# Performance work log

Hardware: AMD Instinct MI355X
Metric: run time of the kernel (lower is better)

The kernel has to match this reference:

```python
import jax, jax.numpy as jnp
import numpy as np

EPS = 1e-5

def _conv(x, w, b):
    # stride-2, pad-1 3x3 conv, NCHW / OIHW
    y = jax.lax.conv_general_dilated(x, w, (2, 2), [(1, 1), (1, 1)],
                                     dimension_numbers=('NCHW', 'OIHW', 'NCHW'))
    return y + b[None, :, None, None]

def _bn(x, gamma, beta):
    # training-mode batchnorm: batch statistics over (N,H,W), biased variance
    mu = x.mean(axis=(0, 2, 3), keepdims=True)
    var = x.var(axis=(0, 2, 3), keepdims=True)
    return gamma[None, :, None, None] * (x - mu) * jax.lax.rsqrt(var + EPS) + beta[None, :, None, None]

def setup_inputs():
    key = jax.random.key(0)
    ks = iter(jax.random.split(key, 40))
    def rn(shape, scale=0.05):
        return jax.random.normal(next(ks), shape, dtype=jnp.float32) * scale
    d = {}
    d['img'] = jax.random.normal(next(ks), (64, 3, 75, 75), dtype=jnp.float32)
    d['qst'] = jax.random.normal(next(ks), (64, 11), dtype=jnp.float32)
    # conv stack 3->32->64->128->256
    d['w1'] = rn((32, 3, 3, 3));    d['b1'] = jnp.zeros((32,), jnp.float32)
    d['w2'] = rn((64, 32, 3, 3));   d['b2'] = jnp.zeros((64,), jnp.float32)
    d['w3'] = rn((128, 64, 3, 3));  d['b3'] = jnp.zeros((128,), jnp.float32)
    d['w4'] = rn((256, 128, 3, 3)); d['b4'] = jnp.zeros((256,), jnp.float32)
    for i, c in zip((1, 2, 3, 4), (32, 64, 128, 256)):
        d[f'g{i}'] = jnp.ones((c,), jnp.float32)
        d[f'be{i}'] = jnp.zeros((c,), jnp.float32)
    # g MLP (torch Linear weights are [out,in])
    d['gw1'] = rn((2000, 523)); d['gb1'] = jnp.zeros((2000,), jnp.float32)
    d['gw2'] = rn((2000, 2000)); d['gb2'] = jnp.zeros((2000,), jnp.float32)
    d['gw3'] = rn((2000, 2000)); d['gb3'] = jnp.zeros((2000,), jnp.float32)
    d['gw4'] = rn((2000, 2000)); d['gb4'] = jnp.zeros((2000,), jnp.float32)
    # f MLP
    d['fw1'] = rn((1000, 2000)); d['fb1'] = jnp.zeros((1000,), jnp.float32)
    d['fw2'] = rn((500, 1000));  d['fb2'] = jnp.zeros((500,), jnp.float32)
    d['fw3'] = rn((100, 500));   d['fb3'] = jnp.zeros((100,), jnp.float32)
    d['fw4'] = rn((10, 100));    d['fb4'] = jnp.zeros((10,), jnp.float32)
    return d

def reference(img, qst, w1, b1, w2, b2, w3, b3, w4, b4,
              g1, be1, g2, be2, g3, be3, g4, be4,
              gw1, gb1, gw2, gb2, gw3, gb3, gw4, gb4,
              fw1, fb1, fw2, fb2, fw3, fb3, fw4, fb4):
    x = jax.nn.relu(_bn(_conv(img, w1, b1), g1, be1))
    x = jax.nn.relu(_bn(_conv(x, w2, b2), g2, be2))
    x = jax.nn.relu(_bn(_conv(x, w3, b3), g3, be3))
    x = jax.nn.relu(_bn(_conv(x, w4, b4), g4, be4))   # [B,256,5,5]
    B = x.shape[0]
    obj = x.reshape(B, 256, 25).transpose(0, 2, 1)     # [B,25,256], row-major like the loop
    oi = jnp.broadcast_to(obj[:, :, None, :], (B, 25, 25, 256))
    oj = jnp.broadcast_to(obj[:, None, :, :], (B, 25, 25, 256))
    q = jnp.broadcast_to(qst[:, None, None, :], (B, 25, 25, 11))
    pairs = jnp.concatenate([oi, oj, q], axis=-1).reshape(B * 625, 523)
    h = jax.nn.relu(pairs @ gw1.T + gb1)
    h = jax.nn.relu(h @ gw2.T + gb2)
    h = jax.nn.relu(h @ gw3.T + gb3)
    h = jax.nn.relu(h @ gw4.T + gb4)
    x_g = h.reshape(B, 625, 2000).sum(axis=1) / 625.0
    x_f = jax.nn.relu(x_g @ fw1.T + fb1)
    x_f = jax.nn.relu(x_f @ fw2.T + fb2)
    x_f = jax.nn.relu(x_f @ fw3.T + fb3)
    x_f = x_f @ fw4.T + fb4
    return jax.nn.log_softmax(x_f, axis=-1)
```

## Files before the change

kernel.cpp:

```cpp
#include <hip/hip_runtime.h>

typedef unsigned short u16;
typedef unsigned int u32;
typedef __attribute__((ext_vector_type(8))) short bf16x8;
typedef __attribute__((ext_vector_type(4))) float f32x4;

#define BN_EPS 1e-5f
#define BN_S 16

__device__ __forceinline__ float bf2f(u16 u) {
  union { unsigned u; float f; } x; x.u = ((unsigned)u) << 16; return x.f;
}
__device__ __forceinline__ u16 f2bf(float f) {
  union { float f; unsigned u; } x; x.f = f;
  unsigned r = x.u + 0x7FFFu + ((x.u >> 16) & 1u);
  return (u16)(r >> 16);
}

__global__ __launch_bounds__(256) void conv1_lds(const float* __restrict__ img,
                                                 const float* __restrict__ w,
                                                 const float* __restrict__ b,
                                                 float* __restrict__ C1) {
  int blk = blockIdx.x;
  int n = blk / 38, ho = blk % 38;
  __shared__ float in_s[9 * 80];
  __shared__ float w_s[32 * 27];
  __shared__ float b_s[32];
  int t = threadIdx.x;
  for (int i = t; i < 720; i += 256) in_s[i] = 0.f;
  __syncthreads();
  for (int i = t; i < 675; i += 256) {
    int wi = i % 75; int q = i / 75; int kh = q % 3; int ci = q / 3;
    int hi = ho * 2 - 1 + kh;
    if (hi >= 0 && hi < 75)
      in_s[(ci * 3 + kh) * 80 + wi + 1] = img[((size_t)(n * 3 + ci) * 75 + hi) * 75 + wi];
  }
  for (int i = t; i < 864; i += 256) w_s[i] = w[i];
  if (t < 32) b_s[t] = b[t];
  __syncthreads();
  for (int idx = t; idx < 1216; idx += 256) {
    int wo = idx >> 5, co = idx & 31;
    float acc = b_s[co];
    const float* wp = w_s + co * 27;
#pragma unroll
    for (int ci = 0; ci < 3; ci++) {
#pragma unroll
      for (int kh = 0; kh < 3; kh++) {
        const float* ip = in_s + (ci * 3 + kh) * 80 + 2 * wo;
        const float* wq = wp + ci * 9 + kh * 3;
        acc += ip[0] * wq[0] + ip[1] * wq[1] + ip[2] * wq[2];
      }
    }
    C1[((size_t)blk * 38 + wo) * 32 + co] = acc;
  }
}

__global__ void bn_partial(const float* __restrict__ C, int ldc, int M,
                           float* __restrict__ part) {
  int c = blockIdx.x; int s = blockIdx.y; int t = threadIdx.x;
  int rowsPer = (M + BN_S - 1) / BN_S;
  int r0 = s * rowsPer; int r1 = r0 + rowsPer; if (r1 > M) r1 = M;
  float s1 = 0.f, s2 = 0.f;
  for (int r = r0 + t; r < r1; r += 256) {
    float v = C[(size_t)r * ldc + c]; s1 += v; s2 += v * v;
  }
  __shared__ float l1[256], l2[256];
  l1[t] = s1; l2[t] = s2; __syncthreads();
  for (int off = 128; off > 0; off >>= 1) {
    if (t < off) { l1[t] += l1[t + off]; l2[t] += l2[t + off]; }
    __syncthreads();
  }
  if (t == 0) { part[s * 512 + c] = l1[0]; part[s * 512 + 256 + c] = l2[0]; }
}

__global__ void bn_final(const float* __restrict__ part, const float* __restrict__ gamma,
                         const float* __restrict__ beta, float* __restrict__ ss,
                         int C, int M) {
  int c = threadIdx.x;
  if (c >= C) { if (c < 256) { ss[c] = 0.f; ss[256 + c] = 0.f; } return; }
  float s1 = 0.f, s2 = 0.f;
#pragma unroll
  for (int s = 0; s < BN_S; s++) { s1 += part[s * 512 + c]; s2 += part[s * 512 + 256 + c]; }
  float mu = s1 / M;
  float var = s2 / M - mu * mu;
  float sc = gamma[c] * rsqrtf(var + BN_EPS);
  ss[c] = sc; ss[256 + c] = beta[c] - mu * sc;
}

__global__ void bnrelu_im2col(const float* __restrict__ Cprev, int ldprev, int Hp, int Wp,
                              const float* __restrict__ ss, u16* __restrict__ X,
                              int Ho, int Wo, int Ci, int Mp) {
  int civ4 = Ci >> 2;
  int idx = blockIdx.x * blockDim.x + threadIdx.x;
  int total = Mp * 9 * civ4;
  if (idx >= total) return;
  int cv = idx % civ4; int t2 = idx / civ4;
  int tap = t2 % 9; int row = t2 / 9;
  int K = 9 * Ci;
  u16* dst = X + (size_t)row * K + tap * Ci + cv * 4;
  int HW = Ho * Wo;
  int Mvalid = 64 * HW;
  ushort4 o4; o4.x = 0; o4.y = 0; o4.z = 0; o4.w = 0;
  if (row < Mvalid) {
    int wo = row % Wo; int t = row / Wo;
    int ho = t % Ho; int n = t / Ho;
    int kh = tap / 3, kw = tap % 3;
    int hi = ho * 2 - 1 + kh, wi = wo * 2 - 1 + kw;
    if (hi >= 0 && hi < Hp && wi >= 0 && wi < Wp) {
      const float* src = Cprev + ((size_t)((n * Hp + hi) * Wp + wi)) * ldprev + cv * 4;
      float4 v = *(const float4*)src;
      int c0 = cv * 4;
      float a;
      a = v.x * ss[c0 + 0] + ss[256 + c0 + 0]; o4.x = f2bf(a > 0.f ? a : 0.f);
      a = v.y * ss[c0 + 1] + ss[256 + c0 + 1]; o4.y = f2bf(a > 0.f ? a : 0.f);
      a = v.z * ss[c0 + 2] + ss[256 + c0 + 2]; o4.z = f2bf(a > 0.f ? a : 0.f);
      a = v.w * ss[c0 + 3] + ss[256 + c0 + 3]; o4.w = f2bf(a > 0.f ? a : 0.f);
    }
  }
  *(ushort4*)dst = o4;
}

__global__ void pack_convw(const float* __restrict__ w, u16* __restrict__ Wp,
                           int Co, int Ci, int Cop) {
  int K = 9 * Ci;
  int idx = blockIdx.x * blockDim.x + threadIdx.x;
  if (idx >= Cop * K) return;
  int k = idx % K; int co = idx / K;
  int tap = k / Ci; int ci = k % Ci;
  float v = (co < Co) ? w[((size_t)co * Ci + ci) * 9 + tap] : 0.f;
  Wp[idx] = f2bf(v);
}

__global__ void pad_bias(const float* __restrict__ b, float* __restrict__ bc, int Co, int Cop) {
  int i = blockIdx.x * blockDim.x + threadIdx.x;
  if (i < Cop) bc[i] = (i < Co) ? b[i] : 0.f;
}

__global__ void obj_from_c4(const float* __restrict__ C4, const float* __restrict__ ss,
                            u16* __restrict__ obj) {
  int idx = blockIdx.x * blockDim.x + threadIdx.x;
  if (idx >= 1664 * 256) return;
  int c = idx & 255; int row = idx >> 8;
  float v = 0.f;
  if (row < 1600) {
    float x = C4[(size_t)row * 256 + c];
    x = x * ss[c] + ss[256 + c];
    v = x > 0.f ? x : 0.f;
  }
  obj[idx] = f2bf(v);
}

__global__ void pack_w1(const float* __restrict__ gw1, u16* __restrict__ W1a, u16* __restrict__ W1b) {
  int idx = blockIdx.x * blockDim.x + threadIdx.x;
  if (idx >= 2048 * 256) return;
  int k = idx & 255, n = idx >> 8;
  float a = 0.f, b = 0.f;
  if (n < 2000) { a = gw1[(size_t)n * 523 + k]; b = gw1[(size_t)n * 523 + 256 + k]; }
  W1a[idx] = f2bf(a); W1b[idx] = f2bf(b);
}

__global__ void pack_wpad(const float* __restrict__ w, u16* __restrict__ Wp,
                          int N, int K, int Np, int Kp) {
  int idx = blockIdx.x * blockDim.x + threadIdx.x;
  if (idx >= Np * Kp) return;
  int k = idx % Kp, n = idx / Kp;
  float v = (n < N && k < K) ? w[(size_t)n * K + k] : 0.f;
  Wp[idx] = f2bf(v);
}

__global__ void pack_bias3(const float* __restrict__ b2, const float* __restrict__ b3,
                           const float* __restrict__ b4, float* __restrict__ bp) {
  int i = blockIdx.x * blockDim.x + threadIdx.x;
  if (i >= 2048) return;
  bp[i]        = (i < 2000) ? b2[i] : 0.f;
  bp[2048 + i] = (i < 2000) ? b3[i] : 0.f;
  bp[4096 + i] = (i < 2000) ? b4[i] : 0.f;
}

__global__ void q_build(const float* __restrict__ qst, const float* __restrict__ gw1,
                        const float* __restrict__ gb1, float* __restrict__ Q) {
  int idx = blockIdx.x * blockDim.x + threadIdx.x;
  if (idx >= 64 * 2048) return;
  int o = idx & 2047, b = idx >> 11;
  float v = 0.f;
  if (o < 2000) {
    v = gb1[o];
    const float* w = gw1 + (size_t)o * 523 + 512;
    const float* q = qst + b * 11;
#pragma unroll
    for (int k = 0; k < 11; k++) v += q[k] * w[k];
  }
  Q[idx] = v;
}

__global__ void pack_xgb(const float* __restrict__ xg, u16* __restrict__ xgb) {
  int idx = blockIdx.x * blockDim.x + threadIdx.x;
  if (idx >= 128 * 2048) return;
  int row = idx >> 11;
  float v = (row < 64) ? xg[idx] * (1.f / 625.f) : 0.f;
  xgb[idx] = f2bf(v);
}

typedef const __attribute__((address_space(1))) u32* gas1;
typedef __attribute__((address_space(3))) u32* las3;
__device__ __forceinline__ void gld16(const void* g, void* l) {
  __builtin_amdgcn_global_load_lds((gas1)g, (las3)l, 16, 0, 0);
}

template <int EPI>
__global__ __launch_bounds__(256) void gemm_bt(
    const u16* __restrict__ A, int lda,
    const u16* __restrict__ W, int ldb,
    float* __restrict__ Cf, u16* __restrict__ Cb, int ldc,
    const float* __restrict__ bias, int KT, int NTN) {
  __shared__ __align__(16) char lds[32768];
  int bid = blockIdx.x;
  int wg;
  if ((gridDim.x & 7) == 0) {
    int cpx = gridDim.x >> 3;
    wg = (bid & 7) * cpx + (bid >> 3);
  } else {
    wg = bid;
  }
  int mt = wg / NTN, nt = wg % NTN;
  int tid = threadIdx.x;
  int wave = tid >> 6, lane = tid & 63;
  int r = lane & 15, g = lane >> 4;
  int wr = wave >> 1, wc = wave & 1;

  const u16* Asrc = A + (size_t)(mt * 128 + wave * 32 + r) * lda + g * 8;
  const u16* Wsrc = W + (size_t)(nt * 128 + wave * 32 + r) * ldb + g * 8;

  f32x4 acc[4][4];
#pragma unroll
  for (int i = 0; i < 4; i++)
#pragma unroll
    for (int j = 0; j < 4; j++) acc[i][j] = (f32x4){0.f, 0.f, 0.f, 0.f};

  {
    char* Al = lds; char* Wl = lds + 8192;
    gld16(Asrc, Al + wave * 2048);
    gld16(Asrc + (size_t)16 * lda, Al + wave * 2048 + 1024);
    gld16(Wsrc, Wl + wave * 2048);
    gld16(Wsrc + (size_t)16 * ldb, Wl + wave * 2048 + 1024);
  }
  __syncthreads();

  int buf = 0;
  for (int kt = 0; kt < KT; kt++) {
    if (kt + 1 < KT) {
      int k0 = (kt + 1) * 32;
      char* Al = lds + (buf ^ 1) * 16384; char* Wl = Al + 8192;
      gld16(Asrc + k0, Al + wave * 2048);
      gld16(Asrc + k0 + (size_t)16 * lda, Al + wave * 2048 + 1024);
      gld16(Wsrc + k0, Wl + wave * 2048);
      gld16(Wsrc + k0 + (size_t)16 * ldb, Wl + wave * 2048 + 1024);
    }
    char* Al = lds + buf * 16384; char* Wl = Al + 8192;
    bf16x8 a[4], w[4];
#pragma unroll
    for (int i = 0; i < 4; i++) a[i] = *(const bf16x8*)(Al + (wr * 4 + i) * 1024 + lane * 16);
#pragma unroll
    for (int j = 0; j < 4; j++) w[j] = *(const bf16x8*)(Wl + (wc * 4 + j) * 1024 + lane * 16);
#pragma unroll
    for (int i = 0; i < 4; i++)
#pragma unroll
      for (int j = 0; j < 4; j++)
        acc[i][j] = __builtin_amdgcn_mfma_f32_16x16x32_bf16(a[i], w[j], acc[i][j], 0, 0, 0);
    __syncthreads();
    buf ^= 1;
  }

  int rowb = mt * 128 + wr * 64 + (lane >> 4) * 4;
  int colb = nt * 128 + wc * 64 + (lane & 15);
#pragma unroll
  for (int i = 0; i < 4; i++) {
#pragma unroll
    for (int j = 0; j < 4; j++) {
      int col = colb + j * 16;
      float bv = (EPI == 2 || EPI == 5) ? bias[col] : 0.f;
#pragma unroll
      for (int q = 0; q < 4; q++) {
        int row = rowb + i * 16 + q;
        float v = acc[i][j][q];
        if (EPI == 2) {
          Cf[(size_t)row * ldc + col] = v + bv;
        } else if (EPI == 3) {
          Cb[(size_t)row * ldc + col] = f2bf(v);
        } else if (EPI == 5) {
          float z = v + bv; z = z > 0.f ? z : 0.f;
          Cb[(size_t)row * ldc + col] = f2bf(z);
        } else {
          Cf[(size_t)row * ldc + col] = v;
        }
      }
    }
  }
}

#define MF16(d, av, bv) d = __builtin_amdgcn_mfma_f32_16x16x32_bf16(av, bv, d, 0, 0, 0)

template <int NT>
__global__ __launch_bounds__(512, 2) void gemm256(
    const u16* __restrict__ A, const u16* __restrict__ W,
    u16* __restrict__ Cb, const float* __restrict__ bias) {
  __shared__ __align__(16) char lds[131072];
  int bid = blockIdx.x;
  int cpx = gridDim.x >> 3;
  int wg = (bid & 7) * cpx + (bid >> 3);
  int mt = wg >> 3, nt = wg & 7;
  int tid = threadIdx.x;
  int wave = tid >> 6, lane = tid & 63;
  int wr = wave >> 2, wc = wave & 3;
  int wcl = wc & 1, wch = wc >> 1;
  int l15 = lane & 15, l7 = lane & 7, lh = lane >> 4;

  int srcChunkOff = (((lane & 7) ^ (lane >> 3)) << 3);
  int srcRowInWave = (lane >> 3);
  auto stageA = [&](int tt, int slot, int h) {
#pragma unroll
    for (int s = 0; s < 2; s++) {
      const u16* src = A + (size_t)(mt * 256 + h * 128 + s * 64 + wave * 8 + srcRowInWave) * 2048
                         + tt * 64 + srcChunkOff;
      gld16(src, lds + slot * 65536 + h * 16384 + s * 8192 + wave * 1024);
    }
  };
  auto stageB = [&](int tt, int slot, int h) {
#pragma unroll
    for (int s = 0; s < 2; s++) {
      const u16* src = W + (size_t)(nt * 256 + h * 128 + s * 64 + wave * 8 + srcRowInWave) * 2048
                         + tt * 64 + srcChunkOff;
      gld16(src, lds + slot * 65536 + 32768 + h * 16384 + s * 8192 + wave * 1024);
    }
  };

  f32x4 acc[8][4];
#pragma unroll
  for (int i = 0; i < 8; i++)
#pragma unroll
    for (int j = 0; j < 4; j++) acc[i][j] = (f32x4){0.f, 0.f, 0.f, 0.f};

  stageA(0, 0, 0); stageA(0, 0, 1); stageB(0, 0, 0); stageB(0, 0, 1);
  stageB(1, 1, 0); stageB(1, 1, 1);
  asm volatile("s_waitcnt vmcnt(4)" ::: "memory");
  __builtin_amdgcn_s_barrier();

  bf16x8 b00, b01, b10, b11, b20, b21, b30, b31;

#define AROFF(Q, i, ks) \
  ((((2 * (Q) + (i)) * 16 + l15) * 128) + (((((ks) * 4) + lh) ^ l7) << 4))
#define BROFF(j, ks) \
  ((((wcl * 4 + (j)) * 16 + l15) * 128) + (((((ks) * 4) + lh) ^ l7) << 4))

#define PHASE(Q, T, BUF)                                                         \
  {                                                                              \
    const char* Ab = lds + (BUF) * 65536 + wr * 16384;                           \
    const char* Bb = lds + (BUF) * 65536 + 32768 + wch * 16384;                  \
    if (Q == 0) {                                                                \
      b00 = *(const bf16x8*)(Bb + BROFF(0, 0));                                  \
      b01 = *(const bf16x8*)(Bb + BROFF(0, 1));                                  \
      b10 = *(const bf16x8*)(Bb + BROFF(1, 0));                                  \
      b11 = *(const bf16x8*)(Bb + BROFF(1, 1));                                  \
      b20 = *(const bf16x8*)(Bb + BROFF(2, 0));                                  \
      b21 = *(const bf16x8*)(Bb + BROFF(2, 1));                                  \
      b30 = *(const bf16x8*)(Bb + BROFF(3, 0));                                  \
      b31 = *(const bf16x8*)(Bb + BROFF(3, 1));                                  \
    }                                                                            \
    bf16x8 a00 = *(const bf16x8*)(Ab + AROFF(Q, 0, 0));                          \
    bf16x8 a01 = *(const bf16x8*)(Ab + AROFF(Q, 0, 1));                          \
    bf16x8 a10 = *(const bf16x8*)(Ab + AROFF(Q, 1, 0));                          \
    bf16x8 a11 = *(const bf16x8*)(Ab + AROFF(Q, 1, 1));                          \
    if (Q == 0) { if ((T) + 1 < NT) stageA((T) + 1, (BUF) ^ 1, 0); }             \
    if (Q == 1) { if ((T) + 1 < NT) stageA((T) + 1, (BUF) ^ 1, 1);               \
                  if ((T) + 2 < NT) stageB((T) + 2, (BUF), 0); }                 \
    if (Q == 2) { if ((T) + 2 < NT) stageB((T) + 2, (BUF), 1); }                 \
    __builtin_amdgcn_s_barrier();                                                \
    __builtin_amdgcn_s_setprio(1);                                               \
    MF16(acc[2 * Q + 0][0], a00, b00); MF16(acc[2 * Q + 0][0], a01, b01);        \
    MF16(acc[2 * Q + 0][1], a00, b10); MF16(acc[2 * Q + 0][1], a01, b11);        \
    MF16(acc[2 * Q + 0][2], a00, b20); MF16(acc[2 * Q + 0][2], a01, b21);        \
    MF16(acc[2 * Q + 0][3], a00, b30); MF16(acc[2 * Q + 0][3], a01, b31);        \
    MF16(acc[2 * Q + 1][0], a10, b00); MF16(acc[2 * Q + 1][0], a11, b01);        \
    MF16(acc[2 * Q + 1][1], a10, b10); MF16(acc[2 * Q + 1][1], a11, b11);        \
    MF16(acc[2 * Q + 1][2], a10, b20); MF16(acc[2 * Q + 1][2], a11, b21);        \
    MF16(acc[2 * Q + 1][3], a10, b30); MF16(acc[2 * Q + 1][3], a11, b31);        \
    __builtin_amdgcn_s_setprio(0);                                               \
    if (Q == 3) { asm volatile("s_waitcnt vmcnt(4)" ::: "memory"); }             \
    __builtin_amdgcn_s_barrier();                                                \
  }

#pragma unroll 1
  for (int t2 = 0; t2 < NT; t2 += 2) {
    PHASE(0, t2, 0) PHASE(1, t2, 0) PHASE(2, t2, 0) PHASE(3, t2, 0)
    PHASE(0, t2 + 1, 1) PHASE(1, t2 + 1, 1) PHASE(2, t2 + 1, 1) PHASE(3, t2 + 1, 1)
  }
#undef PHASE
#undef AROFF
#undef BROFF

  int rowb = mt * 256 + wr * 128 + (lane >> 4) * 4;
  int colb = nt * 256 + wc * 64 + (lane & 15);
#pragma unroll
  for (int i = 0; i < 8; i++) {
#pragma unroll
    for (int j = 0; j < 4; j++) {
      int col = colb + j * 16;
      float bv = bias[col];
#pragma unroll
      for (int q = 0; q < 4; q++) {
        int row = rowb + i * 16 + q;
        float v = acc[i][j][q] + bv;
        v = v > 0.f ? v : 0.f;
        Cb[(size_t)row * 2048 + col] = f2bf(v);
      }
    }
  }
}

__global__ void h1_build(const u16* __restrict__ Af, const u16* __restrict__ Bf,
                         const float* __restrict__ Q, u16* __restrict__ h1,
                         int r0, int nvalid) {
  int lrow = blockIdx.x;
  int t = threadIdx.x;
  u16* dst = h1 + (size_t)lrow * 2048;
  if (lrow >= nvalid) {
#pragma unroll
    for (int it = 0; it < 2; it++) {
      int o = it * 1024 + t * 4;
      ushort4 z; z.x = 0; z.y = 0; z.z = 0; z.w = 0;
      *(ushort4*)(dst + o) = z;
    }
    return;
  }
  int grow = r0 + lrow;
  int b = grow / 625; int rem = grow % 625;
  int i = rem / 25, j = rem % 25;
  const u16* Ap = Af + (size_t)(b * 25 + i) * 2048;
  const u16* Bp = Bf + (size_t)(b * 25 + j) * 2048;
  const float* Qp = Q + (size_t)b * 2048;
#pragma unroll
  for (int it = 0; it < 2; it++) {
    int o = it * 1024 + t * 4;
    ushort4 a4 = *(const ushort4*)(Ap + o);
    ushort4 b4 = *(const ushort4*)(Bp + o);
    float4 qv = *(const float4*)(Qp + o);
    ushort4 outv;
    float v;
    v = bf2f(a4.x) + bf2f(b4.x) + qv.x; outv.x = f2bf(v > 0.f ? v : 0.f);
    v = bf2f(a4.y) + bf2f(b4.y) + qv.y; outv.y = f2bf(v > 0.f ? v : 0.f);
    v = bf2f(a4.z) + bf2f(b4.z) + qv.z; outv.z = f2bf(v > 0.f ? v : 0.f);
    v = bf2f(a4.w) + bf2f(b4.w) + qv.w; outv.w = f2bf(v > 0.f ? v : 0.f);
    *(ushort4*)(dst + o) = outv;
  }
}

__global__ void zero_xg(float* __restrict__ xg) {
  int i = blockIdx.x * blockDim.x + threadIdx.x;
  if (i < 64 * 2048) xg[i] = 0.f;
}

__global__ void reduce_part2(const u16* __restrict__ h4, float* __restrict__ part,
                             int r0, int nvalid, int bfirst) {
  int seg = blockIdx.x; int s = blockIdx.y; int t = threadIdx.x;
  int b = bfirst + seg;
  int lo = b * 625 - r0; if (lo < 0) lo = 0;
  int hi = (b + 1) * 625 - r0; if (hi > nvalid) hi = nvalid;
  int len = hi - lo;
  int k0 = lo + (len * s) / 5;
  int k1 = lo + (len * (s + 1)) / 5;
  const u16* base = h4 + t * 8;
  float a0 = 0.f, a1 = 0.f, a2 = 0.f, a3 = 0.f, a4 = 0.f, a5 = 0.f, a6 = 0.f, a7 = 0.f;
  for (int k = k0; k < k1; k++) {
    uint4 u = *(const uint4*)(base + (size_t)k * 2048);
    a0 += bf2f((u16)(u.x & 0xffff)); a1 += bf2f((u16)(u.x >> 16));
    a2 += bf2f((u16)(u.y & 0xffff)); a3 += bf2f((u16)(u.y >> 16));
    a4 += bf2f((u16)(u.z & 0xffff)); a5 += bf2f((u16)(u.z >> 16));
    a6 += bf2f((u16)(u.w & 0xffff)); a7 += bf2f((u16)(u.w >> 16));
  }
  float* dst = part + ((size_t)(seg * 5 + s) * 2048) + t * 8;
  dst[0] = a0; dst[1] = a1; dst[2] = a2; dst[3] = a3;
  dst[4] = a4; dst[5] = a5; dst[6] = a6; dst[7] = a7;
}

__global__ void reduce_fin2(const float* __restrict__ part, float* __restrict__ xg,
                            int bfirst, int nseg) {
  int idx = blockIdx.x * blockDim.x + threadIdx.x;
  if (idx >= nseg * 2048) return;
  int seg = idx >> 11; int o = idx & 2047;
  float sv = 0.f;
#pragma unroll
  for (int s = 0; s < 5; s++) sv += part[(size_t)(seg * 5 + s) * 2048 + o];
  xg[(size_t)(bfirst + seg) * 2048 + o] += sv;
}

__global__ void f_layer4(const u16* __restrict__ x, const float* __restrict__ Wf,
                         const float* __restrict__ bf_, float* __restrict__ y) {
  int gwid = (blockIdx.x * blockDim.x + threadIdx.x) >> 6;
  int lane = threadIdx.x & 63;
  if (gwid >= 64 * 10) return;
  int b = gwid / 10, o = gwid % 10;
  const u16* xp = x + (size_t)b * 128;
  const float* wp = Wf + (size_t)o * 100;
  float s = 0.f;
  for (int k = lane; k < 100; k += 64) s += bf2f(xp[k]) * wp[k];
  for (int off = 32; off > 0; off >>= 1) s += __shfl_down(s, off);
  if (lane == 0) y[b * 16 + o] = s + bf_[o];
}

__global__ void lsm_kernel(const float* __restrict__ xf4, float* __restrict__ out) {
  int b = blockIdx.x * blockDim.x + threadIdx.x;
  if (b >= 64) return;
  const float* x = xf4 + b * 16;
  float m = x[0];
  for (int i = 1; i < 10; i++) m = fmaxf(m, x[i]);
  float s = 0.f;
  for (int i = 0; i < 10; i++) s += expf(x[i] - m);
  float ls = logf(s);
  for (int i = 0; i < 10; i++) out[b * 10 + i] = x[i] - m - ls;
}

extern "C" void kernel_launch(void* const* d_in, const int* in_sizes, int n_in,
                              void* d_out, int out_size, void* d_ws, size_t ws_size,
                              hipStream_t stream) {
  const float* img = (const float*)d_in[0];
  const float* qst = (const float*)d_in[1];
  const float* w1 = (const float*)d_in[2];  const float* b1 = (const float*)d_in[3];
  const float* w2 = (const float*)d_in[4];  const float* b2 = (const float*)d_in[5];
  const float* w3 = (const float*)d_in[6];  const float* b3 = (const float*)d_in[7];
  const float* w4 = (const float*)d_in[8];  const float* b4 = (const float*)d_in[9];
  const float* g1 = (const float*)d_in[10]; const float* be1 = (const float*)d_in[11];
  const float* g2 = (const float*)d_in[12]; const float* be2 = (const float*)d_in[13];
  const float* g3 = (const float*)d_in[14]; const float* be3 = (const float*)d_in[15];
  const float* g4 = (const float*)d_in[16]; const float* be4 = (const float*)d_in[17];
  const float* gw1 = (const float*)d_in[18]; const float* gb1 = (const float*)d_in[19];
  const float* gw2 = (const float*)d_in[20]; const float* gb2 = (const float*)d_in[21];
  const float* gw3 = (const float*)d_in[22]; const float* gb3 = (const float*)d_in[23];
  const float* gw4 = (const float*)d_in[24]; const float* gb4 = (const float*)d_in[25];
  const float* fw1 = (const float*)d_in[26]; const float* fb1 = (const float*)d_in[27];
  const float* fw2 = (const float*)d_in[28]; const float* fb2 = (const float*)d_in[29];
  const float* fw3 = (const float*)d_in[30]; const float* fb3 = (const float*)d_in[31];
  const float* fw4 = (const float*)d_in[32]; const float* fb4 = (const float*)d_in[33];
  float* out = (float*)d_out;

  char* P = (char*)d_ws;
  auto alloc = [&](size_t bytes) -> char* {
    char* r = P; P += (bytes + 255) & ~(size_t)255; return r;
  };
  u16* Wp2 = (u16*)alloc(2048ull * 2048 * 2);
  u16* Wp3 = (u16*)alloc(2048ull * 2048 * 2);
  u16* Wp4 = (u16*)alloc(2048ull * 2048 * 2);
  u16* Afu = (u16*)alloc(1664ull * 2048 * 2);
  u16* Bfu = (u16*)alloc(1664ull * 2048 * 2);
  float* Q = (float*)alloc(64ull * 2048 * 4);
  float* bp = (float*)alloc(3ull * 2048 * 4);
  float* xg = (float*)alloc(64ull * 2048 * 4);
  u16* obj = (u16*)alloc(1664ull * 256 * 2);
  u16* W1a = (u16*)alloc(2048ull * 256 * 2);
  u16* W1b = (u16*)alloc(2048ull * 256 * 2);
  u16* Fp1 = (u16*)alloc(1024ull * 2048 * 2);
  u16* Fp2 = (u16*)alloc(512ull * 1024 * 2);
  u16* Fp3 = (u16*)alloc(128ull * 512 * 2);
  float* fbc1 = (float*)alloc(1024 * 4);
  float* fbc2 = (float*)alloc(512 * 4);
  float* fbc3 = (float*)alloc(128 * 4);
  u16* xgb  = (u16*)alloc(128ull * 2048 * 2);
  u16* xf1b = (u16*)alloc(128ull * 1024 * 2);
  u16* xf2b = (u16*)alloc(128ull * 512 * 2);
  u16* xf3b = (u16*)alloc(128ull * 128 * 2);
  float* xf4 = (float*)alloc(64ull * 16 * 4);
  u16* h0  = (u16*)alloc(8192ull * 2048 * 2);
  u16* h1b = (u16*)alloc(8192ull * 2048 * 2);
  float* rpart = (float*)alloc(14ull * 5 * 2048 * 4);
  float* C1 = (float*)alloc(92416ull * 32 * 4);
  u16*   X2 = (u16*)alloc(23168ull * 288 * 2);
  float* C2 = (float*)alloc(23168ull * 128 * 4);
  u16*   X3 = (u16*)alloc(6400ull * 576 * 2);
  float* C3 = (float*)alloc(6400ull * 128 * 4);
  u16*   X4 = (u16*)alloc(1664ull * 1152 * 2);
  float* C4 = (float*)alloc(1664ull * 256 * 4);
  u16*  Wc2 = (u16*)alloc(128ull * 288 * 2);
  u16*  Wc3 = (u16*)alloc(128ull * 576 * 2);
  u16*  Wc4 = (u16*)alloc(256ull * 1152 * 2);
  float* bc2 = (float*)alloc(128 * 4);
  float* bc3 = (float*)alloc(128 * 4);
  float* bc4 = (float*)alloc(256 * 4);
  float* bnp = (float*)alloc(BN_S * 512 * 4);
  float* ss  = (float*)alloc(512 * 4);

  pack_convw<<<(128 * 288 + 255) / 256, 256, 0, stream>>>(w2, Wc2, 64, 32, 128);
  pack_convw<<<(128 * 576 + 255) / 256, 256, 0, stream>>>(w3, Wc3, 128, 64, 128);
  pack_convw<<<(256 * 1152 + 255) / 256, 256, 0, stream>>>(w4, Wc4, 256, 128, 256);
  pad_bias<<<1, 256, 0, stream>>>(b2, bc2, 64, 128);
  pad_bias<<<1, 256, 0, stream>>>(b3, bc3, 128, 128);
  pad_bias<<<1, 256, 0, stream>>>(b4, bc4, 256, 256);

  conv1_lds<<<64 * 38, 256, 0, stream>>>(img, w1, b1, C1);
  bn_partial<<<dim3(32, BN_S), 256, 0, stream>>>(C1, 32, 92416, bnp);
  bn_final<<<1, 256, 0, stream>>>(bnp, g1, be1, ss, 32, 92416);
  bnrelu_im2col<<<(23168 * 9 * 8 + 255) / 256, 256, 0, stream>>>(C1, 32, 38, 38, ss, X2, 19, 19, 32, 23168);
  gemm_bt<2><<<181, 256, 0, stream>>>(X2, 288, Wc2, 288, C2, nullptr, 128, bc2, 9, 1);

  bn_partial<<<dim3(64, BN_S), 256, 0, stream>>>(C2, 128, 23104, bnp);
  bn_final<<<1, 256, 0, stream>>>(bnp, g2, be2, ss, 64, 23104);
  bnrelu_im2col<<<(6400 * 9 * 16 + 255) / 256, 256, 0, stream>>>(C2, 128, 19, 19, ss, X3, 10, 10, 64, 6400);
  gemm_bt<2><<<50, 256, 0, stream>>>(X3, 576, Wc3, 576, C3, nullptr, 128, bc3, 18, 1);

  bn_partial<<<dim3(128, BN_S), 256, 0, stream>>>(C3, 128, 6400, bnp);
  bn_final<<<1, 256, 0, stream>>>(bnp, g3, be3, ss, 128, 6400);
  bnrelu_im2col<<<(1664 * 9 * 32 + 255) / 256, 256, 0, stream>>>(C3, 128, 10, 10, ss, X4, 5, 5, 128, 1664);
  gemm_bt<2><<<26, 256, 0, stream>>>(X4, 1152, Wc4, 1152, C4, nullptr, 256, bc4, 36, 2);

  bn_partial<<<dim3(256, BN_S), 256, 0, stream>>>(C4, 256, 1600, bnp);
  bn_final<<<1, 256, 0, stream>>>(bnp, g4, be4, ss, 256, 1600);
  obj_from_c4<<<(1664 * 256 + 255) / 256, 256, 0, stream>>>(C4, ss, obj);

  pack_w1<<<2048, 256, 0, stream>>>(gw1, W1a, W1b);
  pack_wpad<<<(2048 * 2048 + 255) / 256, 256, 0, stream>>>(gw2, Wp2, 2000, 2000, 2048, 2048);
  pack_wpad<<<(2048 * 2048 + 255) / 256, 256, 0, stream>>>(gw3, Wp3, 2000, 2000, 2048, 2048);
  pack_wpad<<<(2048 * 2048 + 255) / 256, 256, 0, stream>>>(gw4, Wp4, 2000, 2000, 2048, 2048);
  pack_bias3<<<8, 256, 0, stream>>>(gb2, gb3, gb4, bp);
  q_build<<<512, 256, 0, stream>>>(qst, gw1, gb1, Q);
  pack_wpad<<<(1024 * 2048 + 255) / 256, 256, 0, stream>>>(fw1, Fp1, 1000, 2000, 1024, 2048);
  pack_wpad<<<(512 * 1024 + 255) / 256, 256, 0, stream>>>(fw2, Fp2, 500, 1000, 512, 1024);
  pack_wpad<<<(128 * 512 + 255) / 256, 256, 0, stream>>>(fw3, Fp3, 100, 500, 128, 512);
  pad_bias<<<4, 256, 0, stream>>>(fb1, fbc1, 1000, 1024);
  pad_bias<<<2, 256, 0, stream>>>(fb2, fbc2, 500, 512);
  pad_bias<<<1, 256, 0, stream>>>(fb3, fbc3, 100, 128);

  gemm_bt<3><<<13 * 16, 256, 0, stream>>>(obj, 256, W1a, 256, nullptr, Afu, 2048, nullptr, 8, 16);
  gemm_bt<3><<<13 * 16, 256, 0, stream>>>(obj, 256, W1b, 256, nullptr, Bfu, 2048, nullptr, 8, 16);

  zero_xg<<<512, 256, 0, stream>>>(xg);
  const int TOTROWS = 64 * 625;
  for (int c = 0; c < 5; c++) {
    int r0 = c * 8192;
    int nvalid = TOTROWS - r0; if (nvalid > 8192) nvalid = 8192;
    h1_build<<<8192, 256, 0, stream>>>(Afu, Bfu, Q, h0, r0, nvalid);
    gemm256<32><<<256, 512, 0, stream>>>(h0, Wp2, h1b, bp);
    gemm256<32><<<256, 512, 0, stream>>>(h1b, Wp3, h0, bp + 2048);
    gemm256<32><<<256, 512, 0, stream>>>(h0, Wp4, h1b, bp + 4096);
    int bfirst = r0 / 625;
    int blast = (r0 + nvalid - 1) / 625;
    int nseg = blast - bfirst + 1;
    reduce_part2<<<dim3(nseg, 5), 256, 0, stream>>>(h1b, rpart, r0, nvalid, bfirst);
    reduce_fin2<<<(nseg * 2048 + 255) / 256, 256, 0, stream>>>(rpart, xg, bfirst, nseg);
  }

  pack_xgb<<<(128 * 2048 + 255) / 256, 256, 0, stream>>>(xg, xgb);
  gemm_bt<5><<<8, 256, 0, stream>>>(xgb, 2048, Fp1, 2048, nullptr, xf1b, 1024, fbc1, 64, 8);
  gemm_bt<5><<<4, 256, 0, stream>>>(xf1b, 1024, Fp2, 1024, nullptr, xf2b, 512, fbc2, 32, 4);
  gemm_bt<5><<<1, 256, 0, stream>>>(xf2b, 512, Fp3, 512, nullptr, xf3b, 128, fbc3, 16, 1);
  f_layer4<<<(64 * 10 * 64 + 255) / 256, 256, 0, stream>>>(xf3b, fw4, fb4, xf4);
  lsm_kernel<<<1, 64, 0, stream>>>(xf4, out);
}
```

Measured before the change: 1.420 ms.

## Fuse per-image row sum into last g-layer GEMM epilogue and enlarge chunks

The last g-MLP GEMM now reduces its output rows into per-image partial sums inside its epilogue, splitting each 256-row tile at the image boundary and reducing across waves through LDS. This removes the write of the layer-4 activations and the separate reduce kernels. The chunk size is also picked from the free workspace (up to all 40960 rows), so the chain runs in fewer, larger launches with more work per GEMM. The cost is a larger activation footprint, an extra LDS reduction with a barrier in the epilogue, and a small finish kernel that scans the tile partials.

```diff
diff --git a/kernel.cpp b/kernel.cpp
--- a/kernel.cpp
+++ b/kernel.cpp
@@ -300,10 +300,11 @@
 
 #define MF16(d, av, bv) d = __builtin_amdgcn_mfma_f32_16x16x32_bf16(av, bv, d, 0, 0, 0)
 
-template <int NT>
+template <int NT, int SUM>
 __global__ __launch_bounds__(512, 2) void gemm256(
     const u16* __restrict__ A, const u16* __restrict__ W,
-    u16* __restrict__ Cb, const float* __restrict__ bias) {
+    u16* __restrict__ Cb, const float* __restrict__ bias,
+    float* __restrict__ rp4, int r0c, int nvalid) {
   __shared__ __align__(16) char lds[131072];
   int bid = blockIdx.x;
   int cpx = gridDim.x >> 3;
@@ -398,22 +399,61 @@
 #undef AROFF
 #undef BROFF
 
-  int rowb = mt * 256 + wr * 128 + (lane >> 4) * 4;
-  int colb = nt * 256 + wc * 64 + (lane & 15);
-#pragma unroll
-  for (int i = 0; i < 8; i++) {
+  int colb = nt * 256 + wc * 64 + l15;
+  if (SUM == 0) {
+    int rowb = mt * 256 + wr * 128 + lh * 4;
+#pragma unroll
+    for (int i = 0; i < 8; i++) {
+#pragma unroll
+      for (int j = 0; j < 4; j++) {
+        int col = colb + j * 16;
+        float bv = bias[col];
+#pragma unroll
+        for (int q = 0; q < 4; q++) {
+          int row = rowb + i * 16 + q;
+          float v = acc[i][j][q] + bv;
+          v = v > 0.f ? v : 0.f;
+          Cb[(size_t)row * 2048 + col] = f2bf(v);
+        }
+      }
+    }
+  } else {
+    int blockRow0 = mt * 256;
+    int bimg = (r0c + blockRow0) / 625;
+    int boundary = (bimg + 1) * 625 - (r0c + blockRow0);
+    float p0[4] = {0.f, 0.f, 0.f, 0.f};
+    float p1[4] = {0.f, 0.f, 0.f, 0.f};
+#pragma unroll
+    for (int i = 0; i < 8; i++) {
+#pragma unroll
+      for (int j = 0; j < 4; j++) {
+        float bv = bias[colb + j * 16];
+#pragma unroll
+        for (int q = 0; q < 4; q++) {
+          int row_local = wr * 128 + lh * 4 + i * 16 + q;
+          float v = acc[i][j][q] + bv;
+          v = v > 0.f ? v : 0.f;
+          if (blockRow0 + row_local >= nvalid) v = 0.f;
+          bool sg1 = row_local >= boundary;
+          p0[j] += sg1 ? 0.f : v;
+          p1[j] += sg1 ? v : 0.f;
+        }
+      }
+    }
+    float* rs = (float*)lds;
+    int contrib = wr * 4 + lh;
 #pragma unroll
     for (int j = 0; j < 4; j++) {
-      int col = colb + j * 16;
-      float bv = bias[col];
-#pragma unroll
-      for (int q = 0; q < 4; q++) {
-        int row = rowb + i * 16 + q;
-        float v = acc[i][j][q] + bv;
-        v = v > 0.f ? v : 0.f;
-        Cb[(size_t)row * 2048 + col] = f2bf(v);
-      }
-    }
+      int colL = wc * 64 + j * 16 + l15;
+      rs[(contrib * 2 + 0) * 256 + colL] = p0[j];
+      rs[(contrib * 2 + 1) * 256 + colL] = p1[j];
+    }
+    __syncthreads();
+    int seg = tid >> 8, colx = tid & 255;
+    float s = 0.f;
+#pragma unroll
+    for (int c8 = 0; c8 < 8; c8++) s += rs[(c8 * 2 + seg) * 256 + colx];
+    rp4[((size_t)(mt * 2 + seg)) * 2048 + nt * 256 + colx] = s;
   }
 }
 
@@ -459,38 +499,18 @@
   if (i < 64 * 2048) xg[i] = 0.f;
 }
 
-__global__ void reduce_part2(const u16* __restrict__ h4, float* __restrict__ part,
-                             int r0, int nvalid, int bfirst) {
-  int seg = blockIdx.x; int s = blockIdx.y; int t = threadIdx.x;
-  int b = bfirst + seg;
-  int lo = b * 625 - r0; if (lo < 0) lo = 0;
-  int hi = (b + 1) * 625 - r0; if (hi > nvalid) hi = nvalid;
-  int len = hi - lo;
-  int k0 = lo + (len * s) / 5;
-  int k1 = lo + (len * (s + 1)) / 5;
-  const u16* base = h4 + t * 8;
-  float a0 = 0.f, a1 = 0.f, a2 = 0.f, a3 = 0.f, a4 = 0.f, a5 = 0.f, a6 = 0.f, a7 = 0.f;
-  for (int k = k0; k < k1; k++) {
-    uint4 u = *(const uint4*)(base + (size_t)k * 2048);
-    a0 += bf2f((u16)(u.x & 0xffff)); a1 += bf2f((u16)(u.x >> 16));
-    a2 += bf2f((u16)(u.y & 0xffff)); a3 += bf2f((u16)(u.y >> 16));
-    a4 += bf2f((u16)(u.z & 0xffff)); a5 += bf2f((u16)(u.z >> 16));
-    a6 += bf2f((u16)(u.w & 0xffff)); a7 += bf2f((u16)(u.w >> 16));
-  }
-  float* dst = part + ((size_t)(seg * 5 + s) * 2048) + t * 8;
-  dst[0] = a0; dst[1] = a1; dst[2] = a2; dst[3] = a3;
-  dst[4] = a4; dst[5] = a5; dst[6] = a6; dst[7] = a7;
-}
-
-__global__ void reduce_fin2(const float* __restrict__ part, float* __restrict__ xg,
-                            int bfirst, int nseg) {
-  int idx = blockIdx.x * blockDim.x + threadIdx.x;
-  if (idx >= nseg * 2048) return;
-  int seg = idx >> 11; int o = idx & 2047;
-  float sv = 0.f;
-#pragma unroll
-  for (int s = 0; s < 5; s++) sv += part[(size_t)(seg * 5 + s) * 2048 + o];
-  xg[(size_t)(bfirst + seg) * 2048 + o] += sv;
+__global__ void l4_fin(const float* __restrict__ rp4, float* __restrict__ xg,
+                       int r0, int bfirst, int mtiles) {
+  int col = blockIdx.x * 256 + threadIdx.x;
+  int b = bfirst + blockIdx.y;
+  if (b > 63) return;
+  float s = 0.f;
+  for (int mt = 0; mt < mtiles; mt++) {
+    int img0 = (r0 + mt * 256) / 625;
+    if (img0 == b)     s += rp4[((size_t)(mt * 2 + 0)) * 2048 + col];
+    if (img0 + 1 == b) s += rp4[((size_t)(mt * 2 + 1)) * 2048 + col];
+  }
+  xg[(size_t)b * 2048 + col] += s;
 }
 
 __global__ void f_layer4(const u16* __restrict__ x, const float* __restrict__ Wf,
@@ -557,6 +577,7 @@
   u16* obj = (u16*)alloc(1664ull * 256 * 2);
   u16* W1a = (u16*)alloc(2048ull * 256 * 2);
   u16* W1b = (u16*)alloc(2048ull * 256 * 2);
+  float* rp4 = (float*)alloc(160ull * 2 * 2048 * 4);
   u16* Fp1 = (u16*)alloc(1024ull * 2048 * 2);
   u16* Fp2 = (u16*)alloc(512ull * 1024 * 2);
   u16* Fp3 = (u16*)alloc(128ull * 512 * 2);
@@ -568,9 +589,6 @@
   u16* xf2b = (u16*)alloc(128ull * 512 * 2);
   u16* xf3b = (u16*)alloc(128ull * 128 * 2);
   float* xf4 = (float*)alloc(64ull * 16 * 4);
-  u16* h0  = (u16*)alloc(8192ull * 2048 * 2);
-  u16* h1b = (u16*)alloc(8192ull * 2048 * 2);
-  float* rpart = (float*)alloc(14ull * 5 * 2048 * 4);
   float* C1 = (float*)alloc(92416ull * 32 * 4);
   u16*   X2 = (u16*)alloc(23168ull * 288 * 2);
   float* C2 = (float*)alloc(23168ull * 128 * 4);
@@ -587,6 +605,15 @@
   float* bnp = (float*)alloc(BN_S * 512 * 4);
   float* ss  = (float*)alloc(512 * 4);
 
+  size_t used = (size_t)(P - (char*)d_ws);
+  size_t remain = (ws_size > used) ? (ws_size - used) : 0;
+  int CHMAX;
+  if (remain >= 2ull * 40960 * 2048 * 2 + 4096)      CHMAX = 40960;
+  else if (remain >= 2ull * 16384 * 2048 * 2 + 4096) CHMAX = 16384;
+  else                                               CHMAX = 8192;
+  u16* h0  = (u16*)alloc((size_t)CHMAX * 2048 * 2);
+  u16* h1b = (u16*)alloc((size_t)CHMAX * 2048 * 2);
+
   pack_convw<<<(128 * 288 + 255) / 256, 256, 0, stream>>>(w2, Wc2, 64, 32, 128);
   pack_convw<<<(128 * 576 + 255) / 256, 256, 0, stream>>>(w3, Wc3, 128, 64, 128);
   pack_convw<<<(256 * 1152 + 255) / 256, 256, 0, stream>>>(w4, Wc4, 256, 128, 256);
@@ -631,19 +658,22 @@
   gemm_bt<3><<<13 * 16, 256, 0, stream>>>(obj, 256, W1b, 256, nullptr, Bfu, 2048, nullptr, 8, 16);
 
   zero_xg<<<512, 256, 0, stream>>>(xg);
-  const int TOTROWS = 64 * 625;
-  for (int c = 0; c < 5; c++) {
-    int r0 = c * 8192;
-    int nvalid = TOTROWS - r0; if (nvalid > 8192) nvalid = 8192;
-    h1_build<<<8192, 256, 0, stream>>>(Afu, Bfu, Q, h0, r0, nvalid);
-    gemm256<32><<<256, 512, 0, stream>>>(h0, Wp2, h1b, bp);
-    gemm256<32><<<256, 512, 0, stream>>>(h1b, Wp3, h0, bp + 2048);
-    gemm256<32><<<256, 512, 0, stream>>>(h0, Wp4, h1b, bp + 4096);
+  const int TOTPAD = 40960;
+  const int TOTROWS = 40000;
+  int r0 = 0;
+  while (r0 < TOTPAD) {
+    int CH = (TOTPAD - r0 >= CHMAX) ? CHMAX : (TOTPAD - r0);
+    int nvalid = TOTROWS - r0; if (nvalid > CH) nvalid = CH; if (nvalid < 0) nvalid = 0;
+    int mtiles = CH / 256;
+    h1_build<<<(unsigned)CH, 256, 0, stream>>>(Afu, Bfu, Q, h0, r0, nvalid);
+    gemm256<32, 0><<<mtiles * 8, 512, 0, stream>>>(h0, Wp2, h1b, bp, nullptr, 0, 0);
+    gemm256<32, 0><<<mtiles * 8, 512, 0, stream>>>(h1b, Wp3, h0, bp + 2048, nullptr, 0, 0);
+    gemm256<32, 1><<<mtiles * 8, 512, 0, stream>>>(h0, Wp4, nullptr, bp + 4096, rp4, r0, nvalid);
     int bfirst = r0 / 625;
-    int blast = (r0 + nvalid - 1) / 625;
+    int blast = (r0 + CH - 1) / 625; if (blast > 63) blast = 63;
     int nseg = blast - bfirst + 1;
-    reduce_part2<<<dim3(nseg, 5), 256, 0, stream>>>(h1b, rpart, r0, nvalid, bfirst);
-    reduce_fin2<<<(nseg * 2048 + 255) / 256, 256, 0, stream>>>(rpart, xg, bfirst, nseg);
+    l4_fin<<<dim3(8, nseg), 256, 0, stream>>>(rp4, xg, r0, bfirst, mtiles);
+    r0 += CH;
   }
 
   pack_xgb<<<(128 * 2048 + 255) / 256, 256, 0, stream>>>(xg, xgb);
```

Result: faster. 1.200 ms (-15.5%).
